# Kernel tuning notes

Measured on AMD Instinct MI355X. Metric: run time of the kernel, lower is better.

Reference implementation:

```python
import jax, jax.numpy as jnp
import numpy as np

D_MODEL = 1024
N_HEADS = 16
ADAPTIVE_TEMP = 1.0
LN_EPS = 1e-5


def _sinusoidal_pe(max_len, d_model):
    pos = np.arange(max_len)[:, None].astype(np.float32)
    div = np.exp(np.arange(0, d_model, 2).astype(np.float32) * (-np.log(10000.0) / d_model))
    pe = np.zeros((max_len, d_model), dtype=np.float32)
    pe[:, 0::2] = np.sin(pos * div)
    pe[:, 1::2] = np.cos(pos * div)
    return jnp.asarray(pe)


def _mlp2(q, w1, b1, w2, b2):
    # Linear(1,h) -> ReLU -> Linear(h,d)
    return jax.nn.relu(q @ w1 + b1) @ w2 + b2


def setup_inputs() -> dict:
    key = jax.random.key(0)
    ks = jax.random.split(key, 24)
    B, T, D = 2, 2048, D_MODEL
    H2 = D // 2
    s = 0.02
    inp = {
        "x": jax.random.normal(ks[0], (B, T, D), jnp.float32),
        "quantile": jax.random.uniform(ks[1], (B, 1), jnp.float32),
        "quantile_importance": jax.random.uniform(ks[2], (100,), jnp.float32),
        "Wq": jax.random.normal(ks[3], (D, D), jnp.float32) * s,
        "bq": jnp.zeros((D,), jnp.float32),
        "Wk": jax.random.normal(ks[4], (D, D), jnp.float32) * s,
        "bk": jnp.zeros((D,), jnp.float32),
        "Wv": jax.random.normal(ks[5], (D, D), jnp.float32) * s,
        "bv": jnp.zeros((D,), jnp.float32),
        "Wo": jax.random.normal(ks[6], (D, D), jnp.float32) * s,
        "bo": jnp.zeros((D,), jnp.float32),
        "qpq_w1": jax.random.normal(ks[7], (1, H2), jnp.float32) * s,
        "qpq_b1": jnp.zeros((H2,), jnp.float32),
        "qpq_w2": jax.random.normal(ks[8], (H2, D), jnp.float32) * s,
        "qpq_b2": jnp.zeros((D,), jnp.float32),
        "qpk_w1": jax.random.normal(ks[9], (1, H2), jnp.float32) * s,
        "qpk_b1": jnp.zeros((H2,), jnp.float32),
        "qpk_w2": jax.random.normal(ks[10], (H2, D), jnp.float32) * s,
        "qpk_b2": jnp.zeros((D,), jnp.float32),
        "qpv_w1": jax.random.normal(ks[11], (1, H2), jnp.float32) * s,
        "qpv_b1": jnp.zeros((H2,), jnp.float32),
        "qpv_w2": jax.random.normal(ks[12], (H2, D), jnp.float32) * s,
        "qpv_b2": jnp.zeros((D,), jnp.float32),
        "ln_g": jnp.ones((D,), jnp.float32),
        "ln_b": jnp.zeros((D,), jnp.float32),
    }
    return inp


def reference(x, quantile, quantile_importance,
              Wq, bq, Wk, bk, Wv, bv, Wo, bo,
              qpq_w1, qpq_b1, qpq_w2, qpq_b2,
              qpk_w1, qpk_b1, qpk_w2, qpk_b2,
              qpv_w1, qpv_b1, qpv_w2, qpv_b2,
              ln_g, ln_b):
    B, T, D = x.shape
    H = N_HEADS
    dk = D // H

    # positional encoding
    x = x + _sinusoidal_pe(T, D)

    # quantile-conditioned embeddings [B, D]
    q_embed = _mlp2(quantile, qpq_w1, qpq_b1, qpq_w2, qpq_b2)
    k_embed = _mlp2(quantile, qpk_w1, qpk_b1, qpk_w2, qpk_b2)
    v_embed = _mlp2(quantile, qpv_w1, qpv_b1, qpv_w2, qpv_b2)

    # importance weight per batch (no-grad buffer lookup)
    buf = jax.lax.stop_gradient(quantile_importance)
    idx = jnp.clip((quantile[:, 0] * 100).astype(jnp.int32), 0, 99)
    mx = buf.max()
    imp = buf[idx]
    imp = jnp.where(mx > 0, imp / mx, imp)  # [B]

    Q = (x @ Wq + bq) + q_embed[:, None, :]
    K = (x @ Wk + bk) + k_embed[:, None, :]
    V = (x @ Wv + bv) + v_embed[:, None, :]

    # [B, H, T, dk]
    Q = Q.reshape(B, T, H, dk).transpose(0, 2, 1, 3)
    K = K.reshape(B, T, H, dk).transpose(0, 2, 1, 3)
    V = V.reshape(B, T, H, dk).transpose(0, 2, 1, 3)

    scores = jnp.einsum('bhtd,bhsd->bhts', Q, K) / jnp.sqrt(jnp.float32(dk))
    scale = 1.0 + imp * ADAPTIVE_TEMP  # [B]
    scores = scores * scale[:, None, None, None]

    attn = jax.nn.softmax(scores, axis=-1)  # dropout is identity at inference
    out = jnp.einsum('bhts,bhsd->bhtd', attn, V)
    out = out.transpose(0, 2, 1, 3).reshape(B, T, D)
    out = out @ Wo + bo

    y = x + out
    mu = y.mean(axis=-1, keepdims=True)
    var = y.var(axis=-1, keepdims=True)
    return (y - mu) / jnp.sqrt(var + LN_EPS) * ln_g + ln_b
```

## Files before the change

### kernel.cpp

```cpp
#include <hip/hip_runtime.h>

#define D 1024
#define T 2048
#define BATCH 2
#define NR 4096
#define NH 16
#define HID 512

typedef unsigned short u16;
typedef unsigned int u32;
typedef float f32x4 __attribute__((ext_vector_type(4)));
typedef __bf16 bf16x8 __attribute__((ext_vector_type(8)));

__device__ __forceinline__ u16 f2bf(float f) {
    union { __bf16 h; u16 u; } c; c.h = (__bf16)f; return c.u;
}

__device__ __forceinline__ void gload16(const u16* g, u16* l) {
    __builtin_amdgcn_global_load_lds(
        (const __attribute__((address_space(1))) unsigned int*)g,
        (__attribute__((address_space(3))) unsigned int*)l,
        16, 0, 0);
}

__global__ __launch_bounds__(256) void k_mlp1(const float* __restrict__ qtl,
        const float* __restrict__ w1q, const float* __restrict__ b1q, const float* __restrict__ w2q,
        const float* __restrict__ w1k, const float* __restrict__ b1k, const float* __restrict__ w2k,
        const float* __restrict__ w1v, const float* __restrict__ b1v, const float* __restrict__ w2v,
        const float* __restrict__ qimp, float* __restrict__ part, float* __restrict__ scl)
{
    int dc = blockIdx.x;
    int jc = blockIdx.y;
    int wb = blockIdx.z;
    int which = wb >> 1, b = wb & 1;
    const float *w1, *b1, *w2;
    if (which == 0)      { w1 = w1q; b1 = b1q; w2 = w2q; }
    else if (which == 1) { w1 = w1k; b1 = b1k; w2 = w2k; }
    else                 { w1 = w1v; b1 = b1v; w2 = w2v; }
    int tid = threadIdx.x;
    __shared__ float h[128];
    if (tid < 128) {
        int j = jc * 128 + tid;
        h[tid] = fmaxf(qtl[b] * w1[j] + b1[j], 0.0f);
    }
    __syncthreads();
    int d = dc * 256 + tid;
    float acc = 0.0f;
    for (int j = 0; j < 128; ++j) acc += h[j] * w2[(size_t)(jc * 128 + j) * D + d];
    part[((size_t)wb * 4 + jc) * D + d] = acc;
    if (dc == 0 && jc == 0 && wb == 0 && tid < BATCH) {
        float mx = qimp[0];
        for (int i = 1; i < 100; ++i) mx = fmaxf(mx, qimp[i]);
        float q = qtl[tid];
        int idx = (int)(q * 100.0f);
        idx = idx < 0 ? 0 : (idx > 99 ? 99 : idx);
        float imp = qimp[idx];
        if (mx > 0.0f) imp /= mx;
        scl[tid] = 1.0f + imp;
    }
}

__global__ __launch_bounds__(256) void k_mlp2(const float* __restrict__ part,
        const float* __restrict__ b2q, const float* __restrict__ b2k, const float* __restrict__ b2v,
        float* __restrict__ embeds)
{
    int dc = blockIdx.x;
    int wb = blockIdx.y;
    int which = wb >> 1;
    const float* b2 = which == 0 ? b2q : which == 1 ? b2k : b2v;
    int d = dc * 256 + threadIdx.x;
    float acc = b2[d];
    #pragma unroll
    for (int jc = 0; jc < 4; ++jc) acc += part[((size_t)wb * 4 + jc) * D + d];
    embeds[(size_t)wb * D + d] = acc;
}

__global__ __launch_bounds__(256) void k_pe(const float* __restrict__ x,
                                            float* __restrict__ xpe, u16* __restrict__ xpeb)
{
    int idx = (blockIdx.x * 256 + threadIdx.x) * 4;
    int d = idx & (D - 1);
    int t = (idx >> 10) & (T - 1);
    const float KL = -0.0089944731946f;
    float ft = (float)t;
    float dv0 = __expf((float)d * KL);
    float dv1 = __expf((float)(d + 2) * KL);
    float a0 = ft * dv0, a1 = ft * dv1;
    float4 xv = *reinterpret_cast<const float4*>(x + idx);
    float4 r;
    r.x = xv.x + __sinf(a0);
    r.y = xv.y + __cosf(a0);
    r.z = xv.z + __sinf(a1);
    r.w = xv.w + __cosf(a1);
    *reinterpret_cast<float4*>(xpe + idx) = r;
    ushort4 o;
    o.x = f2bf(r.x); o.y = f2bf(r.y); o.z = f2bf(r.z); o.w = f2bf(r.w);
    *reinterpret_cast<ushort4*>(xpeb + idx) = o;
}

__global__ __launch_bounds__(256) void k_wconv(const float* __restrict__ Wq, const float* __restrict__ Wk,
                                               const float* __restrict__ Wv, const float* __restrict__ Wo,
                                               u16* __restrict__ Wt)
{
    __shared__ float tile[64][65];
    int z = blockIdx.z;
    const float* W = z == 0 ? Wq : z == 1 ? Wk : z == 2 ? Wv : Wo;
    u16* out = Wt + (size_t)z * D * D;
    int n0 = blockIdx.x * 64, k0 = blockIdx.y * 64;
    int r = threadIdx.x >> 4;
    int c4 = (threadIdx.x & 15) * 4;
    #pragma unroll
    for (int rr = 0; rr < 64; rr += 16) {
        float4 v = *reinterpret_cast<const float4*>(W + (size_t)(k0 + r + rr) * D + n0 + c4);
        tile[r + rr][c4 + 0] = v.x; tile[r + rr][c4 + 1] = v.y;
        tile[r + rr][c4 + 2] = v.z; tile[r + rr][c4 + 3] = v.w;
    }
    __syncthreads();
    #pragma unroll
    for (int rr = 0; rr < 64; rr += 16) {
        ushort4 o;
        o.x = f2bf(tile[c4 + 0][r + rr]);
        o.y = f2bf(tile[c4 + 1][r + rr]);
        o.z = f2bf(tile[c4 + 2][r + rr]);
        o.w = f2bf(tile[c4 + 3][r + rr]);
        *reinterpret_cast<ushort4*>(out + (size_t)(n0 + r + rr) * D + k0 + c4) = o;
    }
}

__device__ __forceinline__ void gemm128(const u16* __restrict__ Ag, const u16* __restrict__ Bg,
                                        int m0, int n0, f32x4 acc[4][4])
{
    __shared__ u16 As[128 * 64];
    __shared__ u16 Bs[128 * 64];
    const int tid = threadIdx.x;
    const int lane = tid & 63, wave = tid >> 6;
    const int wr = wave >> 1, wc = wave & 1;
    #pragma unroll
    for (int i = 0; i < 4; ++i)
        #pragma unroll
        for (int j = 0; j < 4; ++j)
            #pragma unroll
            for (int e = 0; e < 4; ++e) acc[i][j][e] = 0.0f;

    for (int kt = 0; kt < 16; ++kt) {
        __syncthreads();
        #pragma unroll
        for (int c = 0; c < 4; ++c) {
            int ci = c * 256 + tid;
            int row = ci >> 3;
            int sl = (ci & 7) ^ (row & 7);
            gload16(Ag + (size_t)(m0 + row) * D + kt * 64 + sl * 8, As + (size_t)ci * 8);
            gload16(Bg + (size_t)(n0 + row) * D + kt * 64 + sl * 8, Bs + (size_t)ci * 8);
        }
        __syncthreads();
        #pragma unroll
        for (int ks = 0; ks < 2; ++ks) {
            bf16x8 af[4], bfr[4];
            #pragma unroll
            for (int i = 0; i < 4; ++i) {
                int ra = wr * 64 + i * 16 + (lane & 15);
                int sa = ((ks * 4 + (lane >> 4)) ^ (ra & 7));
                af[i] = *reinterpret_cast<const bf16x8*>((const char*)As + ra * 128 + sa * 16);
                int rb = wc * 64 + i * 16 + (lane & 15);
                int sb = ((ks * 4 + (lane >> 4)) ^ (rb & 7));
                bfr[i] = *reinterpret_cast<const bf16x8*>((const char*)Bs + rb * 128 + sb * 16);
            }
            #pragma unroll
            for (int i = 0; i < 4; ++i)
                #pragma unroll
                for (int j = 0; j < 4; ++j)
                    acc[i][j] = __builtin_amdgcn_mfma_f32_16x16x32_bf16(af[i], bfr[j], acc[i][j], 0, 0, 0);
        }
    }
}

__global__ __launch_bounds__(256, 2)
void k_qkv(const u16* __restrict__ A, const u16* __restrict__ Wt,
           const float* __restrict__ bq, const float* __restrict__ bk, const float* __restrict__ bv,
           const float* __restrict__ embeds, const float* __restrict__ scl,
           u16* __restrict__ Qo, u16* __restrict__ Ko, u16* __restrict__ Vt)
{
    int which = blockIdx.z;
    const u16* Bg = Wt + (size_t)which * D * D;
    const float* bias = which == 0 ? bq : which == 1 ? bk : bv;
    const float* emb = embeds + which * (BATCH * D);
    int m0 = blockIdx.x * 128, n0 = blockIdx.y * 128;
    f32x4 acc[4][4];
    gemm128(A, Bg, m0, n0, acc);
    int lane = threadIdx.x & 63, wave = threadIdx.x >> 6;
    int wr = wave >> 1, wc = wave & 1;
    int rowbase = m0 + wr * 64 + ((lane >> 4) << 2);
    int colbase = n0 + wc * 64 + (lane & 15);
    if (which < 2) {
        u16* Out = which == 0 ? Qo : Ko;
        float sc0 = 1.0f, sc1 = 1.0f;
        if (which == 0) { sc0 = scl[0] * 0.125f; sc1 = scl[1] * 0.125f; }
        #pragma unroll
        for (int j = 0; j < 4; ++j) {
            int c = colbase + j * 16;
            float add0 = bias[c] + emb[c];
            float add1 = bias[c] + emb[D + c];
            #pragma unroll
            for (int i = 0; i < 4; ++i) {
                int rb = rowbase + i * 16;
                #pragma unroll
                for (int jj = 0; jj < 4; ++jj) {
                    int r = rb + jj;
                    float v = (r >> 11) ? (acc[i][j][jj] + add1) * sc1
                                        : (acc[i][j][jj] + add0) * sc0;
                    Out[(size_t)r * D + c] = f2bf(v);
                }
            }
        }
    } else {
        #pragma unroll
        for (int j = 0; j < 4; ++j) {
            int c = colbase + j * 16;
            int hh = c >> 6, cc = c & 63;
            float add0 = bias[c] + emb[c];
            float add1 = bias[c] + emb[D + c];
            #pragma unroll
            for (int i = 0; i < 4; ++i) {
                int rb = rowbase + i * 16;
                int bb = rb >> 11;
                int t = rb & (T - 1);
                float add = bb ? add1 : add0;
                ushort4 o;
                o.x = f2bf(acc[i][j][0] + add);
                o.y = f2bf(acc[i][j][1] + add);
                o.z = f2bf(acc[i][j][2] + add);
                o.w = f2bf(acc[i][j][3] + add);
                *reinterpret_cast<ushort4*>(Vt + ((size_t)((bb * NH + hh) * 64 + cc)) * T + t) = o;
            }
        }
    }
}

__global__ __launch_bounds__(512, 2)
void k_attn(const u16* __restrict__ Q, const u16* __restrict__ K, const u16* __restrict__ Vt,
            u16* __restrict__ AO)
{
    __shared__ u16 Ks[128 * 64];
    __shared__ u16 Vs[64 * 128];
    __shared__ u16 Ps[128][136];
    int bh = blockIdx.x;
    int b = bh >> 4, hh = bh & 15;
    int q0 = blockIdx.y * 128;
    int tid = threadIdx.x;
    int lane = tid & 63, wave = tid >> 6;

    bf16x8 qf[2];
    {
        size_t off = (size_t)(b * T + q0 + wave * 16 + (lane & 15)) * D + hh * 64 + ((lane >> 4) << 3);
        qf[0] = *reinterpret_cast<const bf16x8*>(Q + off);
        qf[1] = *reinterpret_cast<const bf16x8*>(Q + off + 32);
    }

    f32x4 o[4];
    float m_run[4], l_run[4];
    #pragma unroll
    for (int j = 0; j < 4; ++j)
        #pragma unroll
        for (int e = 0; e < 4; ++e) o[j][e] = 0.0f;
    #pragma unroll
    for (int jj = 0; jj < 4; ++jj) { m_run[jj] = -1e30f; l_run[jj] = 0.0f; }

    for (int kt = 0; kt < 16; ++kt) {
        __syncthreads();
        #pragma unroll
        for (int c = 0; c < 2; ++c) {
            int ci = c * 512 + tid;
            int row = ci >> 3;
            int sl = (ci & 7) ^ (row & 7);
            gload16(K + (size_t)(b * T + kt * 128 + row) * D + hh * 64 + sl * 8, Ks + (size_t)ci * 8);
            int rowv = ci >> 4;
            int slv = (ci & 15) ^ (rowv & 7);
            gload16(Vt + (size_t)(bh * 64 + rowv) * T + kt * 128 + slv * 8, Vs + (size_t)ci * 8);
        }
        __syncthreads();
        f32x4 s[8];
        #pragma unroll
        for (int ni = 0; ni < 8; ++ni)
            #pragma unroll
            for (int e = 0; e < 4; ++e) s[ni][e] = 0.0f;
        #pragma unroll
        for (int ks = 0; ks < 2; ++ks)
            #pragma unroll
            for (int ni = 0; ni < 8; ++ni) {
                int rk = ni * 16 + (lane & 15);
                int sp = (ks * 4 + (lane >> 4)) ^ (rk & 7);
                bf16x8 kf = *reinterpret_cast<const bf16x8*>((const char*)Ks + rk * 128 + sp * 16);
                s[ni] = __builtin_amdgcn_mfma_f32_16x16x32_bf16(qf[ks], kf, s[ni], 0, 0, 0);
            }
        float mt[4];
        #pragma unroll
        for (int jj = 0; jj < 4; ++jj) {
            float a = fmaxf(fmaxf(s[0][jj], s[1][jj]), fmaxf(s[2][jj], s[3][jj]));
            float c2 = fmaxf(fmaxf(s[4][jj], s[5][jj]), fmaxf(s[6][jj], s[7][jj]));
            mt[jj] = fmaxf(a, c2);
        }
        #pragma unroll
        for (int off = 1; off < 16; off <<= 1)
            #pragma unroll
            for (int jj = 0; jj < 4; ++jj)
                mt[jj] = fmaxf(mt[jj], __shfl_xor(mt[jj], off, 64));
        bool ok = (mt[0] <= m_run[0] + 8.0f) && (mt[1] <= m_run[1] + 8.0f) &&
                  (mt[2] <= m_run[2] + 8.0f) && (mt[3] <= m_run[3] + 8.0f);
        bool skip = __all((int)ok);
        float corr[4];
        if (!skip) {
            #pragma unroll
            for (int jj = 0; jj < 4; ++jj) {
                float mn = fmaxf(m_run[jj], mt[jj]);
                corr[jj] = __expf(m_run[jj] - mn);
                m_run[jj] = mn;
            }
        }
        float psum[4];
        #pragma unroll
        for (int jj = 0; jj < 4; ++jj) psum[jj] = 0.0f;
        #pragma unroll
        for (int ni = 0; ni < 8; ++ni)
            #pragma unroll
            for (int jj = 0; jj < 4; ++jj) {
                float p = __expf(s[ni][jj] - m_run[jj]);
                s[ni][jj] = p;
                psum[jj] += p;
            }
        #pragma unroll
        for (int off = 1; off < 16; off <<= 1)
            #pragma unroll
            for (int jj = 0; jj < 4; ++jj)
                psum[jj] += __shfl_xor(psum[jj], off, 64);
        if (!skip) {
            #pragma unroll
            for (int jj = 0; jj < 4; ++jj)
                l_run[jj] = l_run[jj] * corr[jj] + psum[jj];
            #pragma unroll
            for (int j = 0; j < 4; ++j)
                #pragma unroll
                for (int jj = 0; jj < 4; ++jj)
                    o[j][jj] *= corr[jj];
        } else {
            #pragma unroll
            for (int jj = 0; jj < 4; ++jj) l_run[jj] += psum[jj];
        }
        #pragma unroll
        for (int ni = 0; ni < 8; ++ni)
            #pragma unroll
            for (int jj = 0; jj < 4; ++jj)
                Ps[wave * 16 + ((lane >> 4) << 2) + jj][ni * 16 + (lane & 15)] = f2bf(s[ni][jj]);
        #pragma unroll
        for (int ks2 = 0; ks2 < 4; ++ks2) {
            bf16x8 pa = *reinterpret_cast<const bf16x8*>(
                (const char*)&Ps[wave * 16 + (lane & 15)][0] + ks2 * 64 + ((lane >> 4) << 4));
            #pragma unroll
            for (int j = 0; j < 4; ++j) {
                int rv = j * 16 + (lane & 15);
                int spv = (ks2 * 4 + (lane >> 4)) ^ (rv & 7);
                bf16x8 vf = *reinterpret_cast<const bf16x8*>((const char*)Vs + rv * 256 + spv * 16);
                o[j] = __builtin_amdgcn_mfma_f32_16x16x32_bf16(pa, vf, o[j], 0, 0, 0);
            }
        }
    }
    #pragma unroll
    for (int jj = 0; jj < 4; ++jj) l_run[jj] = 1.0f / l_run[jj];
    #pragma unroll
    for (int j = 0; j < 4; ++j)
        #pragma unroll
        for (int jj = 0; jj < 4; ++jj) {
            size_t off = (size_t)(b * T + q0 + wave * 16 + ((lane >> 4) << 2) + jj) * D + hh * 64 + j * 16 + (lane & 15);
            AO[off] = f2bf(o[j][jj] * l_run[jj]);
        }
}

__global__ __launch_bounds__(256, 2)
void k_ogemm(const u16* __restrict__ A, const u16* __restrict__ Wt,
             const float* __restrict__ bo, const float* __restrict__ xpe,
             float* __restrict__ y)
{
    int m0 = blockIdx.x * 128, n0 = blockIdx.y * 128;
    f32x4 acc[4][4];
    gemm128(A, Wt, m0, n0, acc);
    int lane = threadIdx.x & 63, wave = threadIdx.x >> 6;
    int wr = wave >> 1, wc = wave & 1;
    int rowbase = m0 + wr * 64 + ((lane >> 4) << 2);
    int colbase = n0 + wc * 64 + (lane & 15);
    #pragma unroll
    for (int j = 0; j < 4; ++j) {
        int c = colbase + j * 16;
        float bc = bo[c];
        #pragma unroll
        for (int i = 0; i < 4; ++i) {
            #pragma unroll
            for (int jj = 0; jj < 4; ++jj) {
                int r = rowbase + i * 16 + jj;
                y[(size_t)r * D + c] = acc[i][j][jj] + bc + xpe[(size_t)r * D + c];
            }
        }
    }
}

__global__ __launch_bounds__(256) void k_ln(const float* __restrict__ y, const float* __restrict__ g,
                                            const float* __restrict__ bb, float* __restrict__ out)
{
    int row = blockIdx.x;
    int tid = threadIdx.x;
    const float* yr = y + (size_t)row * D;
    float4 v = *reinterpret_cast<const float4*>(yr + tid * 4);
    float s = v.x + v.y + v.z + v.w;
    float s2 = v.x * v.x + v.y * v.y + v.z * v.z + v.w * v.w;
    #pragma unroll
    for (int off = 1; off < 64; off <<= 1) {
        s += __shfl_xor(s, off, 64);
        s2 += __shfl_xor(s2, off, 64);
    }
    __shared__ float red[8];
    int wave = tid >> 6, lane = tid & 63;
    if (lane == 0) { red[wave] = s; red[4 + wave] = s2; }
    __syncthreads();
    s = red[0] + red[1] + red[2] + red[3];
    s2 = red[4] + red[5] + red[6] + red[7];
    float mu = s * (1.0f / 1024.0f);
    float var = s2 * (1.0f / 1024.0f) - mu * mu;
    float rstd = rsqrtf(var + 1e-5f);
    float4 gv = *reinterpret_cast<const float4*>(g + tid * 4);
    float4 bv = *reinterpret_cast<const float4*>(bb + tid * 4);
    float4 o;
    o.x = (v.x - mu) * rstd * gv.x + bv.x;
    o.y = (v.y - mu) * rstd * gv.y + bv.y;
    o.z = (v.z - mu) * rstd * gv.z + bv.z;
    o.w = (v.w - mu) * rstd * gv.w + bv.w;
    *reinterpret_cast<float4*>(out + (size_t)row * D + tid * 4) = o;
}

extern "C" void kernel_launch(void* const* d_in, const int* in_sizes, int n_in,
                              void* d_out, int out_size, void* d_ws, size_t ws_size,
                              hipStream_t stream)
{
    const float* x    = (const float*)d_in[0];
    const float* qtl  = (const float*)d_in[1];
    const float* qimp = (const float*)d_in[2];
    const float* Wq = (const float*)d_in[3];
    const float* bq = (const float*)d_in[4];
    const float* Wk = (const float*)d_in[5];
    const float* bk = (const float*)d_in[6];
    const float* Wv = (const float*)d_in[7];
    const float* bv = (const float*)d_in[8];
    const float* Wo = (const float*)d_in[9];
    const float* bo = (const float*)d_in[10];
    const float* qpq_w1 = (const float*)d_in[11];
    const float* qpq_b1 = (const float*)d_in[12];
    const float* qpq_w2 = (const float*)d_in[13];
    const float* qpq_b2 = (const float*)d_in[14];
    const float* qpk_w1 = (const float*)d_in[15];
    const float* qpk_b1 = (const float*)d_in[16];
    const float* qpk_w2 = (const float*)d_in[17];
    const float* qpk_b2 = (const float*)d_in[18];
    const float* qpv_w1 = (const float*)d_in[19];
    const float* qpv_b1 = (const float*)d_in[20];
    const float* qpv_w2 = (const float*)d_in[21];
    const float* qpv_b2 = (const float*)d_in[22];
    const float* ln_g = (const float*)d_in[23];
    const float* ln_b = (const float*)d_in[24];
    (void)in_sizes; (void)n_in; (void)out_size; (void)ws_size;

    char* w = (char*)d_ws;
    float* xpe   = (float*)(w);
    u16* xpeb    = (u16*)(w + (16u << 20));
    u16* Wt      = (u16*)(w + (24u << 20));
    u16* Qb      = (u16*)(w + (32u << 20));
    u16* Kb      = (u16*)(w + (40u << 20));
    u16* Vtb     = (u16*)(w + (48u << 20));
    u16* AOb     = (u16*)(w + (56u << 20));
    float* yb    = (float*)(w + (32u << 20));
    float* emb   = (float*)(w + (64u << 20));
    float* scl   = (float*)(w + (64u << 20) + 32768);
    float* part  = (float*)(w + (64u << 20) + 65536);

    k_mlp1<<<dim3(4, 4, 6), 256, 0, stream>>>(qtl,
        qpq_w1, qpq_b1, qpq_w2,
        qpk_w1, qpk_b1, qpk_w2,
        qpv_w1, qpv_b1, qpv_w2,
        qimp, part, scl);
    k_mlp2<<<dim3(4, 6), 256, 0, stream>>>(part, qpq_b2, qpk_b2, qpv_b2, emb);
    k_pe<<<4096, 256, 0, stream>>>(x, xpe, xpeb);
    k_wconv<<<dim3(16, 16, 4), 256, 0, stream>>>(Wq, Wk, Wv, Wo, Wt);
    k_qkv<<<dim3(32, 8, 3), 256, 0, stream>>>(xpeb, Wt, bq, bk, bv, emb, scl, Qb, Kb, Vtb);
    k_attn<<<dim3(32, 16), 512, 0, stream>>>(Qb, Kb, Vtb, AOb);
    k_ogemm<<<dim3(32, 8), 256, 0, stream>>>(AOb, Wt + (size_t)3 * D * D, bo, xpe, yb);
    k_ln<<<4096, 256, 0, stream>>>(yb, ln_g, ln_b, (float*)d_out);
}
```

Before: 182.0 us.

## Double-buffer K/V tiles and keep P in registers in attention kernel

```diff
diff --git a/kernel.cpp b/kernel.cpp
--- a/kernel.cpp
+++ b/kernel.cpp
@@ -9,11 +9,18 @@
 
 typedef unsigned short u16;
 typedef unsigned int u32;
+typedef unsigned long long u64;
 typedef float f32x4 __attribute__((ext_vector_type(4)));
 typedef __bf16 bf16x8 __attribute__((ext_vector_type(8)));
 
 __device__ __forceinline__ u16 f2bf(float f) {
     union { __bf16 h; u16 u; } c; c.h = (__bf16)f; return c.u;
+}
+
+__device__ __forceinline__ u32 cvtpk(float a, float b) {
+    u32 r;
+    asm("v_cvt_pk_bf16_f32 %0, %1, %2" : "=v"(r) : "v"(a), "v"(b));
+    return r;
 }
 
 __device__ __forceinline__ void gload16(const u16* g, u16* l) {
@@ -194,7 +201,10 @@
     if (which < 2) {
         u16* Out = which == 0 ? Qo : Ko;
         float sc0 = 1.0f, sc1 = 1.0f;
-        if (which == 0) { sc0 = scl[0] * 0.125f; sc1 = scl[1] * 0.125f; }
+        if (which == 0) {
+            sc0 = scl[0] * 0.125f * 1.44269504f;
+            sc1 = scl[1] * 0.125f * 1.44269504f;
+        }
         #pragma unroll
         for (int j = 0; j < 4; ++j) {
             int c = colbase + j * 16;
@@ -236,141 +246,148 @@
     }
 }
 
-__global__ __launch_bounds__(512, 2)
+__global__ __launch_bounds__(512, 4)
 void k_attn(const u16* __restrict__ Q, const u16* __restrict__ K, const u16* __restrict__ Vt,
             u16* __restrict__ AO)
 {
-    __shared__ u16 Ks[128 * 64];
-    __shared__ u16 Vs[64 * 128];
-    __shared__ u16 Ps[128][136];
+    __shared__ u16 Ks[2][128 * 64];
+    __shared__ u16 Vs[2][64 * 128];
     int bh = blockIdx.x;
     int b = bh >> 4, hh = bh & 15;
     int q0 = blockIdx.y * 128;
     int tid = threadIdx.x;
-    int lane = tid & 63, wave = tid >> 6;
+    int lane = tid & 63, wave = tid >> 6, g = lane >> 4;
 
     bf16x8 qf[2];
     {
-        size_t off = (size_t)(b * T + q0 + wave * 16 + (lane & 15)) * D + hh * 64 + ((lane >> 4) << 3);
+        size_t off = (size_t)(b * T + q0 + wave * 16 + (lane & 15)) * D + hh * 64 + (g << 3);
         qf[0] = *reinterpret_cast<const bf16x8*>(Q + off);
         qf[1] = *reinterpret_cast<const bf16x8*>(Q + off + 32);
     }
 
     f32x4 o[4];
-    float m_run[4], l_run[4];
     #pragma unroll
     for (int j = 0; j < 4; ++j)
         #pragma unroll
         for (int e = 0; e < 4; ++e) o[j][e] = 0.0f;
-    #pragma unroll
-    for (int jj = 0; jj < 4; ++jj) { m_run[jj] = -1e30f; l_run[jj] = 0.0f; }
+    float m_run = -1e30f, l_run = 0.0f;
+
+    #pragma unroll
+    for (int c = 0; c < 2; ++c) {
+        int ci = c * 512 + tid;
+        int row = ci >> 3;
+        int sl = (ci & 7) ^ (row & 7);
+        gload16(K + (size_t)(b * T + row) * D + hh * 64 + sl * 8, Ks[0] + (size_t)ci * 8);
+        int rowv = ci >> 4;
+        int slv = (ci & 15) ^ (rowv & 7);
+        gload16(Vt + (size_t)(bh * 64 + rowv) * T + slv * 8, Vs[0] + (size_t)ci * 8);
+    }
+    __syncthreads();
 
     for (int kt = 0; kt < 16; ++kt) {
-        __syncthreads();
-        #pragma unroll
-        for (int c = 0; c < 2; ++c) {
-            int ci = c * 512 + tid;
-            int row = ci >> 3;
-            int sl = (ci & 7) ^ (row & 7);
-            gload16(K + (size_t)(b * T + kt * 128 + row) * D + hh * 64 + sl * 8, Ks + (size_t)ci * 8);
-            int rowv = ci >> 4;
-            int slv = (ci & 15) ^ (rowv & 7);
-            gload16(Vt + (size_t)(bh * 64 + rowv) * T + kt * 128 + slv * 8, Vs + (size_t)ci * 8);
-        }
-        __syncthreads();
+        int cur = kt & 1;
+        if (kt < 15) {
+            int t0 = (kt + 1) * 128;
+            #pragma unroll
+            for (int c = 0; c < 2; ++c) {
+                int ci = c * 512 + tid;
+                int row = ci >> 3;
+                int sl = (ci & 7) ^ (row & 7);
+                gload16(K + (size_t)(b * T + t0 + row) * D + hh * 64 + sl * 8, Ks[cur ^ 1] + (size_t)ci * 8);
+                int rowv = ci >> 4;
+                int slv = (ci & 15) ^ (rowv & 7);
+                gload16(Vt + (size_t)(bh * 64 + rowv) * T + t0 + slv * 8, Vs[cur ^ 1] + (size_t)ci * 8);
+            }
+        }
+        const char* Ksc = (const char*)Ks[cur];
+        const char* Vsc = (const char*)Vs[cur];
         f32x4 s[8];
         #pragma unroll
         for (int ni = 0; ni < 8; ++ni)
             #pragma unroll
             for (int e = 0; e < 4; ++e) s[ni][e] = 0.0f;
+        __builtin_amdgcn_s_setprio(1);
         #pragma unroll
         for (int ks = 0; ks < 2; ++ks)
             #pragma unroll
             for (int ni = 0; ni < 8; ++ni) {
                 int rk = ni * 16 + (lane & 15);
-                int sp = (ks * 4 + (lane >> 4)) ^ (rk & 7);
-                bf16x8 kf = *reinterpret_cast<const bf16x8*>((const char*)Ks + rk * 128 + sp * 16);
-                s[ni] = __builtin_amdgcn_mfma_f32_16x16x32_bf16(qf[ks], kf, s[ni], 0, 0, 0);
-            }
-        float mt[4];
-        #pragma unroll
-        for (int jj = 0; jj < 4; ++jj) {
-            float a = fmaxf(fmaxf(s[0][jj], s[1][jj]), fmaxf(s[2][jj], s[3][jj]));
-            float c2 = fmaxf(fmaxf(s[4][jj], s[5][jj]), fmaxf(s[6][jj], s[7][jj]));
-            mt[jj] = fmaxf(a, c2);
-        }
-        #pragma unroll
-        for (int off = 1; off < 16; off <<= 1)
-            #pragma unroll
-            for (int jj = 0; jj < 4; ++jj)
-                mt[jj] = fmaxf(mt[jj], __shfl_xor(mt[jj], off, 64));
-        bool ok = (mt[0] <= m_run[0] + 8.0f) && (mt[1] <= m_run[1] + 8.0f) &&
-                  (mt[2] <= m_run[2] + 8.0f) && (mt[3] <= m_run[3] + 8.0f);
-        bool skip = __all((int)ok);
-        float corr[4];
+                int sp = (ks * 4 + g) ^ (rk & 7);
+                bf16x8 kf = *reinterpret_cast<const bf16x8*>(Ksc + rk * 128 + sp * 16);
+                s[ni] = __builtin_amdgcn_mfma_f32_16x16x32_bf16(kf, qf[ks], s[ni], 0, 0, 0);
+            }
+        __builtin_amdgcn_s_setprio(0);
+        float mt = s[0][0];
+        #pragma unroll
+        for (int ni = 0; ni < 8; ++ni)
+            #pragma unroll
+            for (int e = 0; e < 4; ++e) mt = fmaxf(mt, s[ni][e]);
+        mt = fmaxf(mt, __shfl_xor(mt, 16, 64));
+        mt = fmaxf(mt, __shfl_xor(mt, 32, 64));
+        bool skip = __all((int)(mt <= m_run + 11.0f));
+        float corr = 1.0f;
         if (!skip) {
-            #pragma unroll
-            for (int jj = 0; jj < 4; ++jj) {
-                float mn = fmaxf(m_run[jj], mt[jj]);
-                corr[jj] = __expf(m_run[jj] - mn);
-                m_run[jj] = mn;
-            }
-        }
-        float psum[4];
-        #pragma unroll
-        for (int jj = 0; jj < 4; ++jj) psum[jj] = 0.0f;
+            float mn = fmaxf(m_run, mt);
+            corr = __builtin_exp2f(m_run - mn);
+            m_run = mn;
+        }
+        float psum = 0.0f;
         #pragma unroll
         for (int ni = 0; ni < 8; ++ni)
             #pragma unroll
-            for (int jj = 0; jj < 4; ++jj) {
-                float p = __expf(s[ni][jj] - m_run[jj]);
-                s[ni][jj] = p;
-                psum[jj] += p;
-            }
-        #pragma unroll
-        for (int off = 1; off < 16; off <<= 1)
-            #pragma unroll
-            for (int jj = 0; jj < 4; ++jj)
-                psum[jj] += __shfl_xor(psum[jj], off, 64);
+            for (int e = 0; e < 4; ++e) {
+                float p = __builtin_exp2f(s[ni][e] - m_run);
+                s[ni][e] = p;
+                psum += p;
+            }
+        psum += __shfl_xor(psum, 16, 64);
+        psum += __shfl_xor(psum, 32, 64);
         if (!skip) {
-            #pragma unroll
-            for (int jj = 0; jj < 4; ++jj)
-                l_run[jj] = l_run[jj] * corr[jj] + psum[jj];
+            l_run = l_run * corr + psum;
+            float c4[4];
+            #pragma unroll
+            for (int jr = 0; jr < 4; ++jr)
+                c4[jr] = __shfl(corr, (lane & 48) | (g << 2) | jr, 64);
             #pragma unroll
             for (int j = 0; j < 4; ++j)
                 #pragma unroll
-                for (int jj = 0; jj < 4; ++jj)
-                    o[j][jj] *= corr[jj];
+                for (int jr = 0; jr < 4; ++jr) o[j][jr] *= c4[jr];
         } else {
-            #pragma unroll
-            for (int jj = 0; jj < 4; ++jj) l_run[jj] += psum[jj];
-        }
-        #pragma unroll
-        for (int ni = 0; ni < 8; ++ni)
-            #pragma unroll
-            for (int jj = 0; jj < 4; ++jj)
-                Ps[wave * 16 + ((lane >> 4) << 2) + jj][ni * 16 + (lane & 15)] = f2bf(s[ni][jj]);
-        #pragma unroll
-        for (int ks2 = 0; ks2 < 4; ++ks2) {
-            bf16x8 pa = *reinterpret_cast<const bf16x8*>(
-                (const char*)&Ps[wave * 16 + (lane & 15)][0] + ks2 * 64 + ((lane >> 4) << 4));
+            l_run += psum;
+        }
+        __builtin_amdgcn_s_setprio(1);
+        #pragma unroll
+        for (int kb = 0; kb < 4; ++kb) {
+            union { bf16x8 v; u32 w[4]; } pa;
+            pa.w[0] = cvtpk(s[2 * kb][0], s[2 * kb][1]);
+            pa.w[1] = cvtpk(s[2 * kb][2], s[2 * kb][3]);
+            pa.w[2] = cvtpk(s[2 * kb + 1][0], s[2 * kb + 1][1]);
+            pa.w[3] = cvtpk(s[2 * kb + 1][2], s[2 * kb + 1][3]);
             #pragma unroll
             for (int j = 0; j < 4; ++j) {
                 int rv = j * 16 + (lane & 15);
-                int spv = (ks2 * 4 + (lane >> 4)) ^ (rv & 7);
-                bf16x8 vf = *reinterpret_cast<const bf16x8*>((const char*)Vs + rv * 256 + spv * 16);
-                o[j] = __builtin_amdgcn_mfma_f32_16x16x32_bf16(pa, vf, o[j], 0, 0, 0);
-            }
-        }
-    }
-    #pragma unroll
-    for (int jj = 0; jj < 4; ++jj) l_run[jj] = 1.0f / l_run[jj];
+                int xm = rv & 7;
+                const char* vb = Vsc + rv * 256 + (g & 1) * 8;
+                union { bf16x8 v; u64 d[2]; } vf;
+                vf.d[0] = *reinterpret_cast<const u64*>(vb + (((4 * kb + (g >> 1)) ^ xm) << 4));
+                vf.d[1] = *reinterpret_cast<const u64*>(vb + (((4 * kb + (g >> 1) + 2) ^ xm) << 4));
+                o[j] = __builtin_amdgcn_mfma_f32_16x16x32_bf16(pa.v, vf.v, o[j], 0, 0, 0);
+            }
+        }
+        __builtin_amdgcn_s_setprio(0);
+        __syncthreads();
+    }
+    float linv = 1.0f / l_run;
+    float l4[4];
+    #pragma unroll
+    for (int jr = 0; jr < 4; ++jr)
+        l4[jr] = __shfl(linv, (lane & 48) | (g << 2) | jr, 64);
     #pragma unroll
     for (int j = 0; j < 4; ++j)
         #pragma unroll
-        for (int jj = 0; jj < 4; ++jj) {
-            size_t off = (size_t)(b * T + q0 + wave * 16 + ((lane >> 4) << 2) + jj) * D + hh * 64 + j * 16 + (lane & 15);
-            AO[off] = f2bf(o[j][jj] * l_run[jj]);
+        for (int jr = 0; jr < 4; ++jr) {
+            size_t off = (size_t)(b * T + q0 + wave * 16 + (g << 2) + jr) * D + hh * 64 + j * 16 + (lane & 15);
+            AO[off] = f2bf(o[j][jr] * l4[jr]);
         }
 }
 
```

Measured after the change: 168.9 us. 7.2% less time.
